# Optimization experiments

Hardware: AMD Instinct MI355X
Metric: run time of the kernel (lower is better)

Reference implementation:

```python
import jax, jax.numpy as jnp
import numpy as np

B = 2        # batch size
G = 128      # dense grid extent per axis
N = 200000   # occupied voxels
M = 200000   # query points
C = 128      # feature dim
IGNORE = -1  # ignore_label

# 8 trilinear corner offsets [8,3]
_OFFSETS = jnp.array([[i, j, k] for i in (0, 1) for j in (0, 1) for k in (0, 1)], dtype=jnp.int32)


def setup_inputs() -> dict:
    key = jax.random.key(0)
    k1, k2, k3, k4, k5 = jax.random.split(key, 5)
    xyz = jax.random.randint(k1, (N, 3), 0, G).astype(jnp.int32)
    bids = jnp.sort(jax.random.randint(k2, (N,), 0, B)).astype(jnp.int32)  # sorted batch ids (sparse tensor layout)
    coords = jnp.concatenate([bids[:, None], xyz], axis=1)                 # [N,4]
    features_3d = jax.random.normal(k3, (N, C), dtype=jnp.float32)
    qxyz = jax.random.uniform(k4, (M, 3), minval=0.0, maxval=float(G - 1))
    qb = jnp.sort(jax.random.randint(k5, (M,), 0, B)).astype(jnp.float32)
    query_points = jnp.concatenate([qb[:, None], qxyz], axis=1)            # [M,4]
    return {"features_3d": features_3d, "coords": coords, "query_points": query_points}


def _trilinear(features_3d, coords, query_points):
    bids = coords[:, 0]
    # per-batch coordinate shift (torch.amin per batch)
    shift = jax.ops.segment_min(coords[:, 1:], bids, num_segments=B)       # [B,3]
    c = coords[:, 1:] - shift[bids]                                        # [N,3]
    qb = query_points[:, 0].astype(jnp.int32)                              # [M]
    q = query_points[:, 1:] - shift[qb].astype(query_points.dtype)         # [M,3]

    # dense occupancy grid: voxel row index, IGNORE where empty
    occ = jnp.full((B, G, G, G), IGNORE, dtype=jnp.int32)
    occ = occ.at[bids, c[:, 0], c[:, 1], c[:, 2]].set(jnp.arange(N, dtype=jnp.int32))

    base = jnp.floor(q).astype(jnp.int32)                                  # [M,3]
    frac = q - base.astype(q.dtype)                                        # [M,3]
    corner = base[:, None, :] + _OFFSETS[None]                             # [M,8,3]
    # trilinear weights: prod over dims of frac (offset=1) or 1-frac (offset=0)
    w = jnp.prod(jnp.where(_OFFSETS[None] == 1, frac[:, None, :], 1.0 - frac[:, None, :]), axis=-1)  # [M,8]

    in_bounds = jnp.all((corner >= 0) & (corner < G), axis=-1)             # [M,8]
    cc = jnp.clip(corner, 0, G - 1)
    idx = occ[qb[:, None], cc[..., 0], cc[..., 1], cc[..., 2]]             # [M,8]
    valid = in_bounds & (idx != IGNORE)

    interp_idx = jnp.where(valid, idx, IGNORE)                             # [M,8]
    interp_w = jnp.where(valid, w, 0.0).astype(features_3d.dtype)          # [M,8]

    gathered = features_3d[jnp.maximum(interp_idx, 0)]                     # [M,8,C]
    query_features = jnp.einsum('mk,mkc->mc', interp_w, gathered)          # [M,C]

    # per-voxel accumulated interpolation weight (invalid -> segment N, dropped)
    seg = jnp.where(valid, interp_idx, N).reshape(-1)
    accum_voxel_weights = jax.ops.segment_sum(interp_w.reshape(-1), seg, num_segments=N + 1)[:N]
    return query_features, interp_idx, interp_w, accum_voxel_weights


def reference(features_3d, coords, query_points):
    return _trilinear(features_3d, coords, query_points)
```

## Files before the change

### kernel.cpp

```cpp
#include <hip/hip_runtime.h>

#define NB   2
#define GG   128
#define CC   128

typedef float v4f __attribute__((ext_vector_type(4)));

constexpr int OCC_INTS  = NB * GG * GG * GG;
constexpr int BMP_WORDS = OCC_INTS / 32;

__global__ void __launch_bounds__(256)
init_kernel(unsigned* __restrict__ bmp, float* __restrict__ acc,
            int* __restrict__ shift, int n) {
    const int tid = blockIdx.x * 256 + threadIdx.x;
    const int nth = gridDim.x * 256;
    if (tid < NB * 3) shift[tid] = 0x7FFFFFFF;
    uint4* b4 = (uint4*)bmp;
    for (int i = tid; i < BMP_WORDS / 4; i += nth)
        b4[i] = make_uint4(0u, 0u, 0u, 0u);
    for (int i = tid; i < n; i += nth) acc[i] = 0.0f;
}

__global__ void __launch_bounds__(256)
scatter_kernel(const int4* __restrict__ coords, int* __restrict__ shift,
               int* __restrict__ occ, unsigned* __restrict__ bmp, int n) {
    __shared__ int smin[NB * 3];
    const int tid = threadIdx.x;
    if (tid < NB * 3) smin[tid] = 0x7FFFFFFF;
    __syncthreads();

    const int i = blockIdx.x * 256 + tid;
    int4 c = make_int4(-1, 0x7FFFFFFF, 0x7FFFFFFF, 0x7FFFFFFF);
    if (i < n) {
        c = coords[i];
        const int lin = ((c.x * GG + c.y) * GG + c.z) * GG + c.w;
        atomicMax(&occ[lin], i);
        atomicOr(&bmp[lin >> 5], 1u << (lin & 31));
    }

    int m0 = (c.x == 0) ? c.y : 0x7FFFFFFF;
    int m1 = (c.x == 0) ? c.z : 0x7FFFFFFF;
    int m2 = (c.x == 0) ? c.w : 0x7FFFFFFF;
    int m3 = (c.x == 1) ? c.y : 0x7FFFFFFF;
    int m4 = (c.x == 1) ? c.z : 0x7FFFFFFF;
    int m5 = (c.x == 1) ? c.w : 0x7FFFFFFF;
#pragma unroll
    for (int off = 32; off > 0; off >>= 1) {
        m0 = min(m0, __shfl_xor(m0, off));
        m1 = min(m1, __shfl_xor(m1, off));
        m2 = min(m2, __shfl_xor(m2, off));
        m3 = min(m3, __shfl_xor(m3, off));
        m4 = min(m4, __shfl_xor(m4, off));
        m5 = min(m5, __shfl_xor(m5, off));
    }
    if ((tid & 63) == 0) {
        atomicMin(&smin[0], m0); atomicMin(&smin[1], m1);
        atomicMin(&smin[2], m2); atomicMin(&smin[3], m3);
        atomicMin(&smin[4], m4); atomicMin(&smin[5], m5);
    }
    __syncthreads();
    if (tid < NB * 3) atomicMin(&shift[tid], smin[tid]);
}

__global__ void __launch_bounds__(256)
corner_kernel(const v4f* __restrict__ qpts,
              const int* __restrict__ shift,
              const int* __restrict__ occ,
              const unsigned* __restrict__ bmp,
              float* __restrict__ out_idx,
              float* __restrict__ out_w,
              float* __restrict__ out_acc,
              int2* __restrict__ pairs,
              int* __restrict__ cnt, int mq) {
    const int t = blockIdx.x * 256 + threadIdx.x;
    if (t >= mq * 8) return;
    const int gq   = t >> 3;
    const int cn   = t & 7;
    const int lane = threadIdx.x & 63;

    const int shx0 = shift[0], shy0 = shift[1], shz0 = shift[2];
    const int shx1 = shift[3], shy1 = shift[4], shz1 = shift[5];

    const v4f qp = qpts[gq];
    const int qb = (int)qp.x;
    const int s0 = qb ? shx1 : shx0;
    const int s1 = qb ? shy1 : shy0;
    const int s2 = qb ? shz1 : shz0;
    const float q0 = qp.y - (float)s0, q1 = qp.z - (float)s1,
                q2 = qp.w - (float)s2;
    const float b0 = floorf(q0), b1 = floorf(q1), b2 = floorf(q2);
    const float f0 = q0 - b0, f1 = q1 - b1, f2 = q2 - b2;
    const int oi = (cn >> 2) & 1, oj = (cn >> 1) & 1, ok = cn & 1;
    const int c0 = (int)b0 + oi, c1 = (int)b1 + oj, c2 = (int)b2 + ok;
    const int a0 = c0 + s0, a1 = c1 + s1, a2 = c2 + s2;
    const float w = (oi ? f0 : 1.0f - f0) * (oj ? f1 : 1.0f - f1) *
                    (ok ? f2 : 1.0f - f2);
    const bool inb = c0 >= 0 && c0 < GG && c1 >= 0 && c1 < GG &&
                     c2 >= 0 && c2 < GG && a0 < GG && a1 < GG && a2 < GG;
    const int p0 = min(max(a0, 0), GG - 1);
    const int p1 = min(max(a1, 0), GG - 1);
    const int p2 = min(max(a2, 0), GG - 1);
    const int alin = ((qb * GG + p0) * GG + p1) * GG + p2;
    const unsigned word = bmp[alin >> 5];
    const bool hit = inb && ((word >> (alin & 31)) & 1u);

    int idx = -1;
    if (hit) idx = occ[alin];
    const float fw = (idx != -1) ? w : 0.0f;

    out_idx[t] = (float)idx;
    out_w[t]   = fw;
    if (idx >= 0 && fw != 0.0f) atomicAdd(&out_acc[idx], fw);

    const unsigned long long bal = __ballot(idx >= 0);
    const unsigned grp = (unsigned)((bal >> (lane & 56)) & 0xFFull);
    const int pos = __popc(grp & ((1u << (lane & 7)) - 1u));
    if (idx >= 0) pairs[(size_t)gq * 8 + pos] = make_int2(idx, __float_as_int(fw));
    if (cn == 0) cnt[gq] = __popc(grp);
}

__global__ void __launch_bounds__(256)
gather_kernel(const float* __restrict__ feats,
              const int2* __restrict__ pairs,
              const int* __restrict__ cnt,
              float* __restrict__ out_qf, int mq) {
    const int t  = blockIdx.x * 256 + threadIdx.x;
    const int gq = t >> 5;
    if (gq >= mq) return;
    const int c4 = (threadIdx.x & 31) << 2;

    const int cq = cnt[gq];
    v4f acc = {0.0f, 0.0f, 0.0f, 0.0f};
    for (int j = 0; j < cq; ++j) {
        const int2  pr = pairs[(size_t)gq * 8 + j];
        const float w  = __int_as_float(pr.y);
        const v4f   f  = *(const v4f*)&feats[(size_t)pr.x * CC + c4];
        acc += w * f;
    }
    __builtin_nontemporal_store(acc, (v4f*)&out_qf[(size_t)gq * CC + c4]);
}

extern "C" void kernel_launch(void* const* d_in, const int* in_sizes, int n_in,
                              void* d_out, int out_size, void* d_ws, size_t ws_size,
                              hipStream_t stream) {
    const float* feats  = (const float*)d_in[0];
    const int4*  coords = (const int4*)d_in[1];
    const v4f*   qpts   = (const v4f*)d_in[2];

    const int n  = in_sizes[1] / 4;
    const int mq = in_sizes[2] / 4;

    float* out     = (float*)d_out;
    float* out_qf  = out;
    float* out_idx = out_qf  + (size_t)mq * CC;
    float* out_w   = out_idx + (size_t)mq * 8;
    float* out_acc = out_w   + (size_t)mq * 8;

    char* ws = (char*)d_ws;
    int*      shift = (int*)ws;                                  ws += 256;
    int*      occ   = (int*)ws;                                  ws += (size_t)OCC_INTS * 4;
    unsigned* bmp   = (unsigned*)ws;                             ws += (size_t)BMP_WORDS * 4;
    int2*     pairs = (int2*)ws;                                 ws += (size_t)mq * 8 * sizeof(int2);
    int*      cnt   = (int*)ws;

    init_kernel   <<<512, 256, 0, stream>>>(bmp, out_acc, shift, n);
    scatter_kernel<<<(n + 255) / 256, 256, 0, stream>>>(coords, shift, occ, bmp, n);
    corner_kernel <<<(mq * 8 + 255) / 256, 256, 0, stream>>>(
        qpts, shift, occ, bmp, out_idx, out_w, out_acc, pairs, cnt, mq);
    gather_kernel <<<(mq * 32 + 255) / 256, 256, 0, stream>>>(
        feats, pairs, cnt, out_qf, mq);
}
```

Baseline: 63.80 us.

## Replace dense occupancy grid and bitmap with open-addressing hash table

```diff
diff --git a/kernel.cpp b/kernel.cpp
--- a/kernel.cpp
+++ b/kernel.cpp
@@ -6,24 +6,32 @@
 
 typedef float v4f __attribute__((ext_vector_type(4)));
 
-constexpr int OCC_INTS  = NB * GG * GG * GG;
-constexpr int BMP_WORDS = OCC_INTS / 32;
+#define HASH_BITS 19
+#define HASH_SLOTS (1u << HASH_BITS)
+#define HASH_MASK  (HASH_SLOTS - 1u)
+
+__device__ __forceinline__ unsigned hash_lin(unsigned lin) {
+    return (lin * 0x9E3779B1u) >> (32 - HASH_BITS);
+}
 
 __global__ void __launch_bounds__(256)
-init_kernel(unsigned* __restrict__ bmp, float* __restrict__ acc,
-            int* __restrict__ shift, int n) {
+init_kernel(unsigned* __restrict__ hkey, unsigned* __restrict__ hval,
+            float* __restrict__ acc, int* __restrict__ shift, int n) {
     const int tid = blockIdx.x * 256 + threadIdx.x;
     const int nth = gridDim.x * 256;
     if (tid < NB * 3) shift[tid] = 0x7FFFFFFF;
-    uint4* b4 = (uint4*)bmp;
-    for (int i = tid; i < BMP_WORDS / 4; i += nth)
-        b4[i] = make_uint4(0u, 0u, 0u, 0u);
+    uint4* k4 = (uint4*)hkey;
+    uint4* v4 = (uint4*)hval;
+    for (int i = tid; i < (int)(HASH_SLOTS / 4); i += nth) {
+        k4[i] = make_uint4(0u, 0u, 0u, 0u);
+        v4[i] = make_uint4(0u, 0u, 0u, 0u);
+    }
     for (int i = tid; i < n; i += nth) acc[i] = 0.0f;
 }
 
 __global__ void __launch_bounds__(256)
 scatter_kernel(const int4* __restrict__ coords, int* __restrict__ shift,
-               int* __restrict__ occ, unsigned* __restrict__ bmp, int n) {
+               unsigned* __restrict__ hkey, unsigned* __restrict__ hval, int n) {
     __shared__ int smin[NB * 3];
     const int tid = threadIdx.x;
     if (tid < NB * 3) smin[tid] = 0x7FFFFFFF;
@@ -33,9 +41,17 @@
     int4 c = make_int4(-1, 0x7FFFFFFF, 0x7FFFFFFF, 0x7FFFFFFF);
     if (i < n) {
         c = coords[i];
-        const int lin = ((c.x * GG + c.y) * GG + c.z) * GG + c.w;
-        atomicMax(&occ[lin], i);
-        atomicOr(&bmp[lin >> 5], 1u << (lin & 31));
+        const unsigned lin = ((c.x * GG + c.y) * GG + c.z) * GG + c.w;
+        const unsigned tag = lin + 1u;
+        unsigned s = hash_lin(lin);
+        for (;;) {
+            const unsigned old = atomicCAS(&hkey[s], 0u, tag);
+            if (old == 0u || old == tag) {
+                atomicMax(&hval[s], (unsigned)i + 1u);
+                break;
+            }
+            s = (s + 1u) & HASH_MASK;
+        }
     }
 
     int m0 = (c.x == 0) ? c.y : 0x7FFFFFFF;
@@ -65,8 +81,8 @@
 __global__ void __launch_bounds__(256)
 corner_kernel(const v4f* __restrict__ qpts,
               const int* __restrict__ shift,
-              const int* __restrict__ occ,
-              const unsigned* __restrict__ bmp,
+              const unsigned* __restrict__ hkey,
+              const unsigned* __restrict__ hval,
               float* __restrict__ out_idx,
               float* __restrict__ out_w,
               float* __restrict__ out_acc,
@@ -97,19 +113,23 @@
                     (ok ? f2 : 1.0f - f2);
     const bool inb = c0 >= 0 && c0 < GG && c1 >= 0 && c1 < GG &&
                      c2 >= 0 && c2 < GG && a0 < GG && a1 < GG && a2 < GG;
-    const int p0 = min(max(a0, 0), GG - 1);
-    const int p1 = min(max(a1, 0), GG - 1);
-    const int p2 = min(max(a2, 0), GG - 1);
-    const int alin = ((qb * GG + p0) * GG + p1) * GG + p2;
-    const unsigned word = bmp[alin >> 5];
-    const bool hit = inb && ((word >> (alin & 31)) & 1u);
 
     int idx = -1;
-    if (hit) idx = occ[alin];
+    if (inb) {
+        const unsigned lin = (((unsigned)qb * GG + a0) * GG + a1) * GG + a2;
+        const unsigned tag = lin + 1u;
+        unsigned s = hash_lin(lin);
+        for (;;) {
+            const unsigned k = hkey[s];
+            if (k == 0u) break;
+            if (k == tag) { idx = (int)hval[s] - 1; break; }
+            s = (s + 1u) & HASH_MASK;
+        }
+    }
     const float fw = (idx != -1) ? w : 0.0f;
 
-    out_idx[t] = (float)idx;
-    out_w[t]   = fw;
+    __builtin_nontemporal_store((float)idx, &out_idx[t]);
+    __builtin_nontemporal_store(fw, &out_w[t]);
     if (idx >= 0 && fw != 0.0f) atomicAdd(&out_acc[idx], fw);
 
     const unsigned long long bal = __ballot(idx >= 0);
@@ -157,16 +177,16 @@
     float* out_acc = out_w   + (size_t)mq * 8;
 
     char* ws = (char*)d_ws;
-    int*      shift = (int*)ws;                                  ws += 256;
-    int*      occ   = (int*)ws;                                  ws += (size_t)OCC_INTS * 4;
-    unsigned* bmp   = (unsigned*)ws;                             ws += (size_t)BMP_WORDS * 4;
-    int2*     pairs = (int2*)ws;                                 ws += (size_t)mq * 8 * sizeof(int2);
+    int*      shift = (int*)ws;                          ws += 256;
+    unsigned* hkey  = (unsigned*)ws;                     ws += (size_t)HASH_SLOTS * 4;
+    unsigned* hval  = (unsigned*)ws;                     ws += (size_t)HASH_SLOTS * 4;
+    int2*     pairs = (int2*)ws;                         ws += (size_t)mq * 8 * sizeof(int2);
     int*      cnt   = (int*)ws;
 
-    init_kernel   <<<512, 256, 0, stream>>>(bmp, out_acc, shift, n);
-    scatter_kernel<<<(n + 255) / 256, 256, 0, stream>>>(coords, shift, occ, bmp, n);
+    init_kernel   <<<1024, 256, 0, stream>>>(hkey, hval, out_acc, shift, n);
+    scatter_kernel<<<(n + 255) / 256, 256, 0, stream>>>(coords, shift, hkey, hval, n);
     corner_kernel <<<(mq * 8 + 255) / 256, 256, 0, stream>>>(
-        qpts, shift, occ, bmp, out_idx, out_w, out_acc, pairs, cnt, mq);
+        qpts, shift, hkey, hval, out_idx, out_w, out_acc, pairs, cnt, mq);
     gather_kernel <<<(mq * 32 + 255) / 256, 256, 0, stream>>>(
         feats, pairs, cnt, out_qf, mq);
 }
```

After: 85.05 us. 33.3% more time.

## Process all eight corners per thread with shared bitmap word loads

Applied to the files above, without the earlier changes.

```diff
diff --git a/kernel.cpp b/kernel.cpp
--- a/kernel.cpp
+++ b/kernel.cpp
@@ -72,11 +72,8 @@
               float* __restrict__ out_acc,
               int2* __restrict__ pairs,
               int* __restrict__ cnt, int mq) {
-    const int t = blockIdx.x * 256 + threadIdx.x;
-    if (t >= mq * 8) return;
-    const int gq   = t >> 3;
-    const int cn   = t & 7;
-    const int lane = threadIdx.x & 63;
+    const int gq = blockIdx.x * 256 + threadIdx.x;
+    if (gq >= mq) return;
 
     const int shx0 = shift[0], shy0 = shift[1], shz0 = shift[2];
     const int shx1 = shift[3], shy1 = shift[4], shz1 = shift[5];
@@ -90,33 +87,74 @@
                 q2 = qp.w - (float)s2;
     const float b0 = floorf(q0), b1 = floorf(q1), b2 = floorf(q2);
     const float f0 = q0 - b0, f1 = q1 - b1, f2 = q2 - b2;
-    const int oi = (cn >> 2) & 1, oj = (cn >> 1) & 1, ok = cn & 1;
-    const int c0 = (int)b0 + oi, c1 = (int)b1 + oj, c2 = (int)b2 + ok;
-    const int a0 = c0 + s0, a1 = c1 + s1, a2 = c2 + s2;
-    const float w = (oi ? f0 : 1.0f - f0) * (oj ? f1 : 1.0f - f1) *
-                    (ok ? f2 : 1.0f - f2);
-    const bool inb = c0 >= 0 && c0 < GG && c1 >= 0 && c1 < GG &&
-                     c2 >= 0 && c2 < GG && a0 < GG && a1 < GG && a2 < GG;
-    const int p0 = min(max(a0, 0), GG - 1);
-    const int p1 = min(max(a1, 0), GG - 1);
-    const int p2 = min(max(a2, 0), GG - 1);
-    const int alin = ((qb * GG + p0) * GG + p1) * GG + p2;
-    const unsigned word = bmp[alin >> 5];
-    const bool hit = inb && ((word >> (alin & 31)) & 1u);
-
-    int idx = -1;
-    if (hit) idx = occ[alin];
-    const float fw = (idx != -1) ? w : 0.0f;
-
-    out_idx[t] = (float)idx;
-    out_w[t]   = fw;
-    if (idx >= 0 && fw != 0.0f) atomicAdd(&out_acc[idx], fw);
-
-    const unsigned long long bal = __ballot(idx >= 0);
-    const unsigned grp = (unsigned)((bal >> (lane & 56)) & 0xFFull);
-    const int pos = __popc(grp & ((1u << (lane & 7)) - 1u));
-    if (idx >= 0) pairs[(size_t)gq * 8 + pos] = make_int2(idx, __float_as_int(fw));
-    if (cn == 0) cnt[gq] = __popc(grp);
+    const int i0 = (int)b0, i1 = (int)b1, i2 = (int)b2;
+
+    const bool vx0 = (i0 >= 0)     && (i0 < GG)     && (i0 + s0 < GG);
+    const bool vx1 = (i0 + 1 >= 0) && (i0 + 1 < GG) && (i0 + 1 + s0 < GG);
+    const bool vy0 = (i1 >= 0)     && (i1 < GG)     && (i1 + s1 < GG);
+    const bool vy1 = (i1 + 1 >= 0) && (i1 + 1 < GG) && (i1 + 1 + s1 < GG);
+    const bool vz0 = (i2 >= 0)     && (i2 < GG)     && (i2 + s2 < GG);
+    const bool vz1 = (i2 + 1 >= 0) && (i2 + 1 < GG) && (i2 + 1 + s2 < GG);
+
+    const int ax0 = min(max(i0 + s0, 0), GG - 1);
+    const int ax1 = min(max(i0 + 1 + s0, 0), GG - 1);
+    const int ay0 = min(max(i1 + s1, 0), GG - 1);
+    const int ay1 = min(max(i1 + 1 + s1, 0), GG - 1);
+    const int az0 = min(max(i2 + s2, 0), GG - 1);
+    const int az1 = min(max(i2 + 1 + s2, 0), GG - 1);
+
+    unsigned pb[8];
+    int      rowbase[4];
+    {
+#define PAIRBITS(P, AXC, AYC, VX, VY)                                          \
+        {                                                                      \
+            const unsigned base = (((unsigned)qb * GG + (AXC)) * GG + (AYC)) * GG; \
+            rowbase[P] = (int)base;                                            \
+            const unsigned lin = base + (unsigned)az0;                         \
+            const unsigned wdi = lin >> 5, bp = lin & 31u;                     \
+            const unsigned wd  = bmp[wdi];                                     \
+            unsigned hi = 0u;                                                  \
+            if (bp == 31u && ((VX) && (VY) && vz1)) hi = bmp[wdi + 1u];        \
+            pb[(P)]     = (wd >> bp) & 1u;                                     \
+            pb[(P) + 4] = (bp < 31u) ? ((wd >> (bp + 1)) & 1u) : (hi & 1u);    \
+        }
+        PAIRBITS(0, ax0, ay0, vx0, vy0)
+        PAIRBITS(1, ax0, ay1, vx0, vy1)
+        PAIRBITS(2, ax1, ay0, vx1, vy0)
+        PAIRBITS(3, ax1, ay1, vx1, vy1)
+#undef PAIRBITS
+    }
+
+    float idxf[8], wout[8];
+    int   pos = 0;
+#pragma unroll
+    for (int cn = 0; cn < 8; ++cn) {
+        const int oi = (cn >> 2) & 1, oj = (cn >> 1) & 1, ok = cn & 1;
+        const float w = (oi ? f0 : 1.0f - f0) *
+                        (oj ? f1 : 1.0f - f1) *
+                        (ok ? f2 : 1.0f - f2);
+        const bool valid = (oi ? vx1 : vx0) && (oj ? vy1 : vy0) &&
+                           (ok ? vz1 : vz0);
+        const int  pair  = oi * 2 + oj;
+        const bool hit   = valid && (pb[pair + 4 * ok] != 0u);
+        int idx = -1;
+        if (hit) idx = occ[rowbase[pair] + (ok ? az1 : az0)];
+        const float fw = hit ? w : 0.0f;
+        idxf[cn] = (float)idx;
+        wout[cn] = fw;
+        if (hit && fw != 0.0f) atomicAdd(&out_acc[idx], fw);
+        if (hit) { pairs[(size_t)gq * 8 + pos] = make_int2(idx, __float_as_int(fw)); ++pos; }
+    }
+    cnt[gq] = pos;
+
+    const v4f vi0 = {idxf[0], idxf[1], idxf[2], idxf[3]};
+    const v4f vi1 = {idxf[4], idxf[5], idxf[6], idxf[7]};
+    const v4f vw0 = {wout[0], wout[1], wout[2], wout[3]};
+    const v4f vw1 = {wout[4], wout[5], wout[6], wout[7]};
+    __builtin_nontemporal_store(vi0, (v4f*)&out_idx[(size_t)gq * 8]);
+    __builtin_nontemporal_store(vi1, (v4f*)&out_idx[(size_t)gq * 8 + 4]);
+    __builtin_nontemporal_store(vw0, (v4f*)&out_w[(size_t)gq * 8]);
+    __builtin_nontemporal_store(vw1, (v4f*)&out_w[(size_t)gq * 8 + 4]);
 }
 
 __global__ void __launch_bounds__(256)
@@ -157,15 +195,15 @@
     float* out_acc = out_w   + (size_t)mq * 8;
 
     char* ws = (char*)d_ws;
-    int*      shift = (int*)ws;                                  ws += 256;
-    int*      occ   = (int*)ws;                                  ws += (size_t)OCC_INTS * 4;
-    unsigned* bmp   = (unsigned*)ws;                             ws += (size_t)BMP_WORDS * 4;
-    int2*     pairs = (int2*)ws;                                 ws += (size_t)mq * 8 * sizeof(int2);
+    int*      shift = (int*)ws;                          ws += 256;
+    int*      occ   = (int*)ws;                          ws += (size_t)OCC_INTS * 4;
+    unsigned* bmp   = (unsigned*)ws;                     ws += (size_t)BMP_WORDS * 4;
+    int2*     pairs = (int2*)ws;                         ws += (size_t)mq * 8 * sizeof(int2);
     int*      cnt   = (int*)ws;
 
     init_kernel   <<<512, 256, 0, stream>>>(bmp, out_acc, shift, n);
     scatter_kernel<<<(n + 255) / 256, 256, 0, stream>>>(coords, shift, occ, bmp, n);
-    corner_kernel <<<(mq * 8 + 255) / 256, 256, 0, stream>>>(
+    corner_kernel <<<(mq + 255) / 256, 256, 0, stream>>>(
         qpts, shift, occ, bmp, out_idx, out_w, out_acc, pairs, cnt, mq);
     gather_kernel <<<(mq * 32 + 255) / 256, 256, 0, stream>>>(
         feats, pairs, cnt, out_qf, mq);
```

Measured after the change: 67.59 us. 1.06x slower.
